# Optimization experiments

Measured on AMD Instinct MI355X. Metric: run time of the kernel, lower is better.

Reference implementation:

```python
import jax, jax.numpy as jnp
import numpy as np
from jax import lax

D_MODEL = 768
N_LAYER = 4
VOCAB = 50280  # 50277 padded to multiple of 8
D_INNER = 2 * D_MODEL
D_STATE = 16
D_CONV = 4
DT_RANK = 48  # ceil(768/16)
EPS = 1e-5


def setup_inputs() -> dict:
    key = jax.random.key(0)
    ks = iter(jax.random.split(key, 16))
    s = 0.02
    B, L = 1, 1024
    inp = {
        "input_ids": jax.random.randint(next(ks), (B, L), 0, 50277, dtype=jnp.int64).astype(jnp.int32),
        "embedding": jax.random.normal(next(ks), (VOCAB, D_MODEL), jnp.float32) * s,
        "in_proj_w": jax.random.normal(next(ks), (N_LAYER, 2 * D_INNER, D_MODEL), jnp.float32) * s,
        "conv_w": jax.random.normal(next(ks), (N_LAYER, D_INNER, 1, D_CONV), jnp.float32) * s,
        "conv_b": jnp.zeros((N_LAYER, D_INNER), jnp.float32),
        "x_proj_w": jax.random.normal(next(ks), (N_LAYER, DT_RANK + 2 * D_STATE, D_INNER), jnp.float32) * s,
        "dt_proj_w": jax.random.normal(next(ks), (N_LAYER, D_INNER, DT_RANK), jnp.float32) * s,
        "dt_proj_b": jax.random.uniform(next(ks), (N_LAYER, D_INNER), jnp.float32, -4.0, -2.0),
        "A_log": jnp.log(jnp.broadcast_to(jnp.arange(1, D_STATE + 1, dtype=jnp.float32), (N_LAYER, D_INNER, D_STATE))),
        "D_param": jnp.ones((N_LAYER, D_INNER), jnp.float32),
        "out_proj_w": jax.random.normal(next(ks), (N_LAYER, D_MODEL, D_INNER), jnp.float32) * s,
        "norm_w": jnp.ones((N_LAYER, D_MODEL), jnp.float32),
        "norm_f_w": jnp.ones((D_MODEL,), jnp.float32),
    }
    return inp


def rmsnorm(x, w):
    var = jnp.mean(jnp.square(x), axis=-1, keepdims=True)
    return x * lax.rsqrt(var + EPS) * w


def silu(x):
    return x * jax.nn.sigmoid(x)


def mamba_mixer(h, in_w, cw, cb, xw, dtw, dtb, A_log, Dp, ow):
    B, L, _ = h.shape
    xz = jnp.einsum("bld,ed->ble", h, in_w)          # [B,L,2*d_inner]
    x, z = jnp.split(xz, 2, axis=-1)
    # causal depthwise conv1d over length
    xc = lax.conv_general_dilated(
        x.transpose(0, 2, 1), cw, (1,), [(D_CONV - 1, 0)],
        dimension_numbers=("NCH", "OIH", "NCH"), feature_group_count=D_INNER,
    ).transpose(0, 2, 1) + cb                          # [B,L,d_inner]
    xc = silu(xc)
    dbl = jnp.einsum("bld,ed->ble", xc, xw)            # [B,L,R+2N]
    dt = jax.nn.softplus(jnp.einsum("blr,dr->bld", dbl[..., :DT_RANK], dtw) + dtb)
    Bm = dbl[..., DT_RANK:DT_RANK + D_STATE]           # [B,L,N]
    Cm = dbl[..., DT_RANK + D_STATE:]                  # [B,L,N]
    A = -jnp.exp(A_log)                                # [d_inner,N]
    dA = jnp.exp(dt[..., None] * A)                    # [B,L,d_inner,N]
    dBx = dt[..., None] * Bm[:, :, None, :] * xc[..., None]

    def step(s, inp):
        a, b, c = inp
        s = a * s + b
        y = jnp.einsum("bdn,bn->bd", s, c)
        return s, y

    s0 = jnp.zeros((B, D_INNER, D_STATE), h.dtype)
    _, ys = lax.scan(step, s0, (dA.transpose(1, 0, 2, 3), dBx.transpose(1, 0, 2, 3), Cm.transpose(1, 0, 2)))
    y = ys.transpose(1, 0, 2) + xc * Dp                # [B,L,d_inner]
    y = y * silu(z)
    return jnp.einsum("ble,de->bld", y, ow)


def reference(input_ids, embedding, in_proj_w, conv_w, conv_b, x_proj_w,
              dt_proj_w, dt_proj_b, A_log, D_param, out_proj_w, norm_w, norm_f_w):
    h = embedding[input_ids]                           # [B,L,D]
    for i in range(N_LAYER):
        h = h + mamba_mixer(rmsnorm(h, norm_w[i]), in_proj_w[i], conv_w[i], conv_b[i],
                            x_proj_w[i], dt_proj_w[i], dt_proj_b[i], A_log[i],
                            D_param[i], out_proj_w[i])
    h = rmsnorm(h, norm_f_w)
    logits = jnp.einsum("bld,vd->blv", h, embedding)   # tied lm_head
    return logits
```

## Files before the change

kernel.cpp:

```cpp
#include <hip/hip_runtime.h>
#include <cstdint>
#include <cstddef>

#define N_LAYER 4
#define VOCABSZ 50280
#define VOCABPAD 50304
#define DMODEL 768
#define DINNER 1536
#define DSTATE 16
#define DTRANK 48
#define SEQL 1024

typedef __bf16 bf16x8 __attribute__((ext_vector_type(8)));
typedef unsigned short us8 __attribute__((ext_vector_type(8)));
typedef float f32x4 __attribute__((ext_vector_type(4)));

__device__ __forceinline__ unsigned short f2bf(float f) {
    unsigned int u = __builtin_bit_cast(unsigned int, f);
    u = (u + 0x7FFFu + ((u >> 16) & 1u)) >> 16;
    return (unsigned short)u;
}

__device__ __forceinline__ void glds16(const unsigned short* g, unsigned short* l) {
    __builtin_amdgcn_global_load_lds(
        (const __attribute__((address_space(1))) void*)g,
        (__attribute__((address_space(3))) void*)l, 16, 0, 0);
}

__global__ __launch_bounds__(256) void cvt_bf16_kernel(
    const float* __restrict__ src, unsigned short* __restrict__ dst, int n8)
{
    int i = blockIdx.x * 256 + threadIdx.x;
    if (i >= n8) return;
    const float4* s = (const float4*)src + (size_t)i * 2;
    float4 a = s[0], b = s[1];
    us8 o = { f2bf(a.x), f2bf(a.y), f2bf(a.z), f2bf(a.w),
              f2bf(b.x), f2bf(b.y), f2bf(b.z), f2bf(b.w) };
    *(us8*)(dst + (size_t)i * 8) = o;
}

__global__ __launch_bounds__(256) void cvt_xw_kernel(
    const float* __restrict__ xw, unsigned short* __restrict__ xwB)
{
    int g = blockIdx.x * 256 + threadIdx.x;
    if (g >= N_LAYER * 128 * 192) return;
    int row = g / 192;
    int c8  = g % 192;
    int layer = row >> 7;
    int r = row & 127;
    us8 o;
    if (r < 80) {
        const float4* s = (const float4*)(xw + ((size_t)(layer * 80 + r) * DINNER) + c8 * 8);
        float4 a = s[0], b = s[1];
        o = (us8){ f2bf(a.x), f2bf(a.y), f2bf(a.z), f2bf(a.w),
                   f2bf(b.x), f2bf(b.y), f2bf(b.z), f2bf(b.w) };
    } else {
        o = (us8){0, 0, 0, 0, 0, 0, 0, 0};
    }
    *(us8*)(xwB + (size_t)row * DINNER + c8 * 8) = o;
}

__device__ __forceinline__ void gemm_compute32(
    const unsigned short* sAbuf, const unsigned short* sBbuf,
    int wm, int wn, int frs, f32x4 (&acc)[4][4])
{
    bf16x8 af[4], bfr[4];
#pragma unroll
    for (int t = 0; t < 4; ++t) {
        af[t]  = __builtin_bit_cast(bf16x8, *(const us8*)&sAbuf[(wm + t * 16) * 32 + frs]);
        bfr[t] = __builtin_bit_cast(bf16x8, *(const us8*)&sBbuf[(wn + t * 16) * 32 + frs]);
    }
#pragma unroll
    for (int mt = 0; mt < 4; ++mt)
#pragma unroll
        for (int nt = 0; nt < 4; ++nt)
            acc[mt][nt] = __builtin_amdgcn_mfma_f32_16x16x32_bf16(
                af[mt], bfr[nt], acc[mt][nt], 0, 0, 0);
}

template <int ADD>
__device__ __forceinline__ void gemm_bf_body(
    const unsigned short* __restrict__ A, const unsigned short* __restrict__ B,
    const float* __restrict__ ADDSRC, float* __restrict__ C, int N, int K)
{
    __shared__ unsigned short sA0[128 * 32];
    __shared__ unsigned short sA1[128 * 32];
    __shared__ unsigned short sB0[128 * 32];
    __shared__ unsigned short sB1[128 * 32];

    const int tid  = threadIdx.x;
    const int lane = tid & 63;
    const int wave = tid >> 6;
    const int wm = (wave & 1) * 64;
    const int wn = (wave >> 1) * 64;
    const int bid = blockIdx.x;
    const int cpx = (int)gridDim.x >> 3;
    const int swz = (bid & 7) * cpx + (bid >> 3);
    const int bm = (swz & 7) << 7;
    const int bn = (swz >> 3) << 7;

    const int scol = ((tid & 3) ^ ((tid >> 3) & 3)) * 8;
    const unsigned short* Ag0 = A + (size_t)(bm + (tid >> 2)) * K + scol;
    const unsigned short* Ag1 = Ag0 + (size_t)64 * K;
    const unsigned short* Bg0 = B + (size_t)(bn + (tid >> 2)) * K + scol;
    const unsigned short* Bg1 = Bg0 + (size_t)64 * K;
    unsigned short* lA0a = sA0 + tid * 8;  unsigned short* lA0b = lA0a + 2048;
    unsigned short* lA1a = sA1 + tid * 8;  unsigned short* lA1b = lA1a + 2048;
    unsigned short* lB0a = sB0 + tid * 8;  unsigned short* lB0b = lB0a + 2048;
    unsigned short* lB1a = sB1 + tid * 8;  unsigned short* lB1b = lB1a + 2048;

    f32x4 acc[4][4];
#pragma unroll
    for (int i = 0; i < 4; ++i)
#pragma unroll
        for (int j = 0; j < 4; ++j) acc[i][j] = (f32x4){0.f, 0.f, 0.f, 0.f};

    const int frs = (lane & 15) * 32 + (((lane >> 4) ^ ((lane >> 1) & 3))) * 8;

    glds16(Ag0, lA0a); glds16(Ag1, lA0b);
    glds16(Bg0, lB0a); glds16(Bg1, lB0b);
    Ag0 += 32; Ag1 += 32; Bg0 += 32; Bg1 += 32;
    __syncthreads();

    for (int k0 = 0; k0 < K; k0 += 64) {
        glds16(Ag0, lA1a); glds16(Ag1, lA1b);
        glds16(Bg0, lB1a); glds16(Bg1, lB1b);
        Ag0 += 32; Ag1 += 32; Bg0 += 32; Bg1 += 32;
        gemm_compute32(sA0, sB0, wm, wn, frs, acc);
        __syncthreads();

        if (k0 + 64 < K) {
            glds16(Ag0, lA0a); glds16(Ag1, lA0b);
            glds16(Bg0, lB0a); glds16(Bg1, lB0b);
            Ag0 += 32; Ag1 += 32; Bg0 += 32; Bg1 += 32;
        }
        gemm_compute32(sA1, sB1, wm, wn, frs, acc);
        __syncthreads();
    }

    const int cn = lane & 15;
    const int cm = (lane >> 4) * 4;
#pragma unroll
    for (int mt = 0; mt < 4; ++mt) {
#pragma unroll
        for (int nt = 0; nt < 4; ++nt) {
            int n = bn + wn + nt * 16 + cn;
            if (n < N) {
#pragma unroll
                for (int r = 0; r < 4; ++r) {
                    int m = bm + wm + mt * 16 + cm + r;
                    size_t idx = (size_t)m * N + n;
                    float v = acc[mt][nt][r];
                    if constexpr (ADD) v += ADDSRC[idx];
                    C[idx] = v;
                }
            }
        }
    }
}

__global__ __launch_bounds__(256) void gemm_in_kernel(
    const unsigned short* __restrict__ A, const unsigned short* __restrict__ B,
    float* __restrict__ C, int N, int K)
{ gemm_bf_body<0>(A, B, nullptr, C, N, K); }

__global__ __launch_bounds__(256) void gemm_out_kernel(
    const unsigned short* __restrict__ A, const unsigned short* __restrict__ B,
    const float* __restrict__ ADDSRC, float* __restrict__ C, int N, int K)
{ gemm_bf_body<1>(A, B, ADDSRC, C, N, K); }

__global__ __launch_bounds__(256) void gemm_xproj_kernel(
    const unsigned short* __restrict__ A, const unsigned short* __restrict__ B,
    float* __restrict__ C, int N, int K)
{ gemm_bf_body<0>(A, B, nullptr, C, N, K); }

__global__ __launch_bounds__(256) void gemm_logits_kernel(
    const unsigned short* __restrict__ A, const unsigned short* __restrict__ B,
    float* __restrict__ C, int N, int K)
{ gemm_bf_body<0>(A, B, nullptr, C, N, K); }

template <int ADD>
__global__ __launch_bounds__(256) void gemm_fb_kernel(
    const float* __restrict__ A, const float* __restrict__ B,
    const float* __restrict__ ADDSRC, float* __restrict__ C,
    int N, int K)
{
    __shared__ unsigned short sA[128 * 40];
    __shared__ unsigned short sB[128 * 40];
    const int tid  = threadIdx.x;
    const int lane = tid & 63;
    const int wave = tid >> 6;
    const int wm = (wave & 1) * 64;
    const int wn = (wave >> 1) * 64;
    const int bm = blockIdx.y * 128;
    const int bn = blockIdx.x * 128;
    const int srow = tid >> 1;
    const int scol = (tid & 1) * 16;
    const float* Ap = A + (size_t)(bm + srow) * K + scol;
    const int brow  = bn + srow;
    const bool bvalid = brow < N;
    const float* Bp = B + (size_t)(bvalid ? brow : 0) * K + scol;
    f32x4 acc[4][4];
#pragma unroll
    for (int i = 0; i < 4; ++i)
#pragma unroll
        for (int j = 0; j < 4; ++j) acc[i][j] = (f32x4){0.f, 0.f, 0.f, 0.f};
    unsigned short* sAp = &sA[srow * 40 + scol];
    unsigned short* sBp = &sB[srow * 40 + scol];
    const int fr = (lane & 15) * 40 + (lane >> 4) * 8;
    for (int k0 = 0; k0 < K; k0 += 32) {
        float4 a0 = *(const float4*)(Ap + k0);
        float4 a1 = *(const float4*)(Ap + k0 + 4);
        float4 a2 = *(const float4*)(Ap + k0 + 8);
        float4 a3 = *(const float4*)(Ap + k0 + 12);
        float4 b0, b1, b2, b3;
        if (bvalid) {
            b0 = *(const float4*)(Bp + k0);
            b1 = *(const float4*)(Bp + k0 + 4);
            b2 = *(const float4*)(Bp + k0 + 8);
            b3 = *(const float4*)(Bp + k0 + 12);
        } else {
            b0 = make_float4(0.f, 0.f, 0.f, 0.f);
            b1 = b0; b2 = b0; b3 = b0;
        }
        __syncthreads();
        us8 va0 = { f2bf(a0.x), f2bf(a0.y), f2bf(a0.z), f2bf(a0.w),
                    f2bf(a1.x), f2bf(a1.y), f2bf(a1.z), f2bf(a1.w) };
        us8 va1 = { f2bf(a2.x), f2bf(a2.y), f2bf(a2.z), f2bf(a2.w),
                    f2bf(a3.x), f2bf(a3.y), f2bf(a3.z), f2bf(a3.w) };
        us8 vb0 = { f2bf(b0.x), f2bf(b0.y), f2bf(b0.z), f2bf(b0.w),
                    f2bf(b1.x), f2bf(b1.y), f2bf(b1.z), f2bf(b1.w) };
        us8 vb1 = { f2bf(b2.x), f2bf(b2.y), f2bf(b2.z), f2bf(b2.w),
                    f2bf(b3.x), f2bf(b3.y), f2bf(b3.z), f2bf(b3.w) };
        *(us8*)(sAp)     = va0;
        *(us8*)(sAp + 8) = va1;
        *(us8*)(sBp)     = vb0;
        *(us8*)(sBp + 8) = vb1;
        __syncthreads();
        bf16x8 af[4], bfr[4];
#pragma unroll
        for (int t = 0; t < 4; ++t) {
            af[t]  = __builtin_bit_cast(bf16x8, *(const us8*)&sA[wm * 40 + t * 640 + fr]);
            bfr[t] = __builtin_bit_cast(bf16x8, *(const us8*)&sB[wn * 40 + t * 640 + fr]);
        }
#pragma unroll
        for (int mt = 0; mt < 4; ++mt)
#pragma unroll
            for (int nt = 0; nt < 4; ++nt)
                acc[mt][nt] = __builtin_amdgcn_mfma_f32_16x16x32_bf16(
                    af[mt], bfr[nt], acc[mt][nt], 0, 0, 0);
    }
    const int cn = lane & 15;
    const int cm = (lane >> 4) * 4;
#pragma unroll
    for (int mt = 0; mt < 4; ++mt) {
#pragma unroll
        for (int nt = 0; nt < 4; ++nt) {
            int n = bn + wn + nt * 16 + cn;
            if (n < N) {
#pragma unroll
                for (int r = 0; r < 4; ++r) {
                    int m = bm + wm + mt * 16 + cm + r;
                    size_t idx = (size_t)m * N + n;
                    float v = acc[mt][nt][r];
                    if constexpr (ADD) v += ADDSRC[idx];
                    C[idx] = v;
                }
            }
        }
    }
}

__global__ __launch_bounds__(256) void embed_kernel(
    const int* __restrict__ ids, const float* __restrict__ emb, float* __restrict__ h)
{
    int l = blockIdx.x;
    int id = ids[l];
    const float* src = emb + (size_t)id * DMODEL;
    for (int d = threadIdx.x; d < DMODEL; d += 256) h[(size_t)l * DMODEL + d] = src[d];
}

template <typename OT>
__global__ __launch_bounds__(256) void rmsnorm_kernel(
    const float* __restrict__ x, const float* __restrict__ w,
    OT* __restrict__ out, int D)
{
    int l = blockIdx.x;
    const float* xr = x + (size_t)l * D;
    float ss = 0.f;
    for (int d = threadIdx.x; d < D; d += 256) { float v = xr[d]; ss += v * v; }
#pragma unroll
    for (int off = 32; off > 0; off >>= 1) ss += __shfl_down(ss, off, 64);
    __shared__ float red[4];
    __shared__ float invs;
    if ((threadIdx.x & 63) == 0) red[threadIdx.x >> 6] = ss;
    __syncthreads();
    if (threadIdx.x == 0)
        invs = rsqrtf((red[0] + red[1] + red[2] + red[3]) / (float)D + 1e-5f);
    __syncthreads();
    float inv = invs;
    for (int d = threadIdx.x; d < D; d += 256) {
        float v = xr[d] * inv * w[d];
        if constexpr (sizeof(OT) == 2) out[(size_t)l * D + d] = f2bf(v);
        else                           out[(size_t)l * D + d] = v;
    }
}

__global__ __launch_bounds__(256) void conv_silu_kernel(
    const float* __restrict__ xz, const float* __restrict__ cw,
    const float* __restrict__ cb, float* __restrict__ xc,
    unsigned short* __restrict__ xcB)
{
    int l = blockIdx.x / 6;
    int d = (blockIdx.x % 6) * 256 + threadIdx.x;
    float w0 = cw[d * 4], w1 = cw[d * 4 + 1], w2 = cw[d * 4 + 2], w3 = cw[d * 4 + 3];
    float acc = cb[d];
    if (l >= 3) acc += xz[(size_t)(l - 3) * 3072 + d] * w0;
    if (l >= 2) acc += xz[(size_t)(l - 2) * 3072 + d] * w1;
    if (l >= 1) acc += xz[(size_t)(l - 1) * 3072 + d] * w2;
    acc += xz[(size_t)l * 3072 + d] * w3;
    float sig = 1.f / (1.f + __expf(-acc));
    float v = acc * sig;
    size_t idx = (size_t)l * DINNER + d;
    xc[idx]  = v;
    xcB[idx] = f2bf(v);
}

__global__ __launch_bounds__(256) void xproj_kernel(
    const float* __restrict__ xc, const float* __restrict__ xw, float* __restrict__ dbl)
{
    int l = blockIdx.x;
    __shared__ float sx[DINNER];
    for (int d = threadIdx.x; d < DINNER; d += 256) sx[d] = xc[(size_t)l * DINNER + d];
    __syncthreads();
    int wave = threadIdx.x >> 6, lane = threadIdx.x & 63;
    for (int e = wave * 20; e < wave * 20 + 20; ++e) {
        const float* wr = xw + (size_t)e * DINNER;
        float s = 0.f;
        for (int d = lane; d < DINNER; d += 64) s += sx[d] * wr[d];
#pragma unroll
        for (int off = 32; off > 0; off >>= 1) s += __shfl_down(s, off, 64);
        if (lane == 0) dbl[l * 80 + e] = s;
    }
}

__global__ __launch_bounds__(256) void dtproj_kernel(
    const float* __restrict__ dbl, const float* __restrict__ dtw,
    const float* __restrict__ dtb, float* __restrict__ dt)
{
    int l = blockIdx.x / 6;
    int e = (blockIdx.x % 6) * 256 + threadIdx.x;
    __shared__ float sd[48];
    if (threadIdx.x < 48) sd[threadIdx.x] = dbl[l * 80 + threadIdx.x];
    __syncthreads();
    float a = dtb[e];
    const float4* wr = (const float4*)(dtw + (size_t)e * 48);
#pragma unroll
    for (int q = 0; q < 12; ++q) {
        float4 w4 = wr[q];
        a += sd[q * 4] * w4.x + sd[q * 4 + 1] * w4.y + sd[q * 4 + 2] * w4.z + sd[q * 4 + 3] * w4.w;
    }
    dt[(size_t)l * DINNER + e] = (a > 20.f) ? a : log1pf(__expf(a));
}

template <typename OT>
__global__ __launch_bounds__(64) void scan_kernel(
    const float* __restrict__ dt, const float* __restrict__ dbl,
    const float* __restrict__ xc, const float* __restrict__ xz,
    const float* __restrict__ alog, const float* __restrict__ dpar,
    OT* __restrict__ yf)
{
    int d0 = blockIdx.x * 4;
    int lane = threadIdx.x;
    int n = lane & 15;
    int dloc = lane >> 4;
    int d = d0 + dloc;
    float A = -__expf(alog[d * 16 + n]);
    float Dq[4];
#pragma unroll
    for (int q = 0; q < 4; ++q) Dq[q] = dpar[d0 + q];

    __shared__ float sdt[64][4];
    __shared__ float sxc[64][4];
    __shared__ float sz[64][4];
    __shared__ float sB[64][16];
    __shared__ float sC[64][16];
    __shared__ float pp[4][64][17];

    float s = 0.f;
    for (int c0 = 0; c0 < SEQL; c0 += 64) {
        int l = c0 + lane;
        *(float4*)&sdt[lane][0] = *(const float4*)&dt[(size_t)l * DINNER + d0];
        *(float4*)&sxc[lane][0] = *(const float4*)&xc[(size_t)l * DINNER + d0];
        *(float4*)&sz[lane][0]  = *(const float4*)&xz[(size_t)l * 3072 + DINNER + d0];
#pragma unroll
        for (int q = 0; q < 4; ++q) {
            *(float4*)&sB[lane][q * 4] = *(const float4*)&dbl[l * 80 + 48 + q * 4];
            *(float4*)&sC[lane][q * 4] = *(const float4*)&dbl[l * 80 + 64 + q * 4];
        }
        __syncthreads();
#pragma unroll 4
        for (int j = 0; j < 64; ++j) {
            float dtv = sdt[j][dloc];
            float xv  = sxc[j][dloc];
            float a = __expf(dtv * A);
            s = fmaf(a, s, dtv * sB[j][n] * xv);
            pp[dloc][j][n] = s * sC[j][n];
        }
        __syncthreads();
#pragma unroll
        for (int q = 0; q < 4; ++q) {
            float accv = 0.f;
#pragma unroll
            for (int nn = 0; nn < 16; ++nn) accv += pp[q][lane][nn];
            float xv = sxc[lane][q];
            float zv = sz[lane][q];
            float sig = 1.f / (1.f + __expf(-zv));
            float v = (accv + xv * Dq[q]) * (zv * sig);
            if constexpr (sizeof(OT) == 2) yf[(size_t)(c0 + lane) * DINNER + d0 + q] = f2bf(v);
            else                           yf[(size_t)(c0 + lane) * DINNER + d0 + q] = v;
        }
        __syncthreads();
    }
}

extern "C" void kernel_launch(void* const* d_in, const int* in_sizes, int n_in,
                              void* d_out, int out_size, void* d_ws, size_t ws_size,
                              hipStream_t stream)
{
    const int*   ids  = (const int*)d_in[0];
    const float* emb  = (const float*)d_in[1];
    const float* inw  = (const float*)d_in[2];
    const float* cw   = (const float*)d_in[3];
    const float* cb   = (const float*)d_in[4];
    const float* xw   = (const float*)d_in[5];
    const float* dtw  = (const float*)d_in[6];
    const float* dtb  = (const float*)d_in[7];
    const float* alog = (const float*)d_in[8];
    const float* dpar = (const float*)d_in[9];
    const float* ow   = (const float*)d_in[10];
    const float* nw   = (const float*)d_in[11];
    const float* nfw  = (const float*)d_in[12];
    float* out = (float*)d_out;

    const size_t MAIN_WS = 138936320ull;

    if (ws_size >= MAIN_WS) {
        char* p = (char*)d_ws;
        float* h    = (float*)p;                 p += (size_t)SEQL * DMODEL * 4;
        float* xz   = (float*)p;                 p += (size_t)SEQL * 3072 * 4;
        float* xc   = (float*)p;                 p += (size_t)SEQL * DINNER * 4;
        float* dbl  = (float*)p;                 p += (size_t)SEQL * 80 * 4;
        float* dt   = (float*)p;                 p += (size_t)SEQL * DINNER * 4;
        unsigned short* xnB  = (unsigned short*)p; p += (size_t)SEQL * DMODEL * 2;
        unsigned short* yfB  = (unsigned short*)p; p += (size_t)SEQL * DINNER * 2;
        unsigned short* embB = (unsigned short*)p; p += (size_t)VOCABPAD * DMODEL * 2;
        unsigned short* inwB = (unsigned short*)p; p += (size_t)N_LAYER * 3072 * DMODEL * 2;
        unsigned short* owB  = (unsigned short*)p; p += (size_t)N_LAYER * DMODEL * DINNER * 2;

        unsigned short* xwB = (unsigned short*)out;
        unsigned short* xcB = xwB + (size_t)N_LAYER * 128 * DINNER;

        int n8;
        n8 = VOCABSZ * DMODEL / 8;
        cvt_bf16_kernel<<<(n8 + 255) / 256, 256, 0, stream>>>(emb, embB, n8);
        n8 = N_LAYER * 3072 * DMODEL / 8;
        cvt_bf16_kernel<<<(n8 + 255) / 256, 256, 0, stream>>>(inw, inwB, n8);
        n8 = N_LAYER * DMODEL * DINNER / 8;
        cvt_bf16_kernel<<<(n8 + 255) / 256, 256, 0, stream>>>(ow, owB, n8);
        cvt_xw_kernel<<<(N_LAYER * 128 * 192 + 255) / 256, 256, 0, stream>>>(xw, xwB);

        embed_kernel<<<SEQL, 256, 0, stream>>>(ids, emb, h);

        for (int i = 0; i < N_LAYER; ++i) {
            rmsnorm_kernel<unsigned short><<<SEQL, 256, 0, stream>>>(
                h, nw + (size_t)i * DMODEL, xnB, DMODEL);
            gemm_in_kernel<<<8 * (3072 / 128), 256, 0, stream>>>(
                xnB, inwB + (size_t)i * 3072 * DMODEL, xz, 3072, DMODEL);
            conv_silu_kernel<<<SEQL * 6, 256, 0, stream>>>(
                xz, cw + (size_t)i * DINNER * 4, cb + (size_t)i * DINNER, xc, xcB);
            gemm_xproj_kernel<<<8, 256, 0, stream>>>(
                xcB, xwB + (size_t)i * 128 * DINNER, dbl, 80, DINNER);
            dtproj_kernel<<<SEQL * 6, 256, 0, stream>>>(
                dbl, dtw + (size_t)i * DINNER * DTRANK, dtb + (size_t)i * DINNER, dt);
            scan_kernel<unsigned short><<<DINNER / 4, 64, 0, stream>>>(
                dt, dbl, xc, xz, alog + (size_t)i * DINNER * DSTATE,
                dpar + (size_t)i * DINNER, yfB);
            gemm_out_kernel<<<8 * (DMODEL / 128), 256, 0, stream>>>(
                yfB, owB + (size_t)i * DMODEL * DINNER, h, h, DMODEL, DINNER);
        }

        rmsnorm_kernel<unsigned short><<<SEQL, 256, 0, stream>>>(h, nfw, xnB, DMODEL);
        gemm_logits_kernel<<<8 * ((VOCABSZ + 127) / 128), 256, 0, stream>>>(
            xnB, embB, out, VOCABSZ, DMODEL);
    } else {
        float* h   = (float*)d_ws;
        float* xn  = h  + (size_t)SEQL * DMODEL;
        float* xz  = xn + (size_t)SEQL * DMODEL;
        float* xc  = xz + (size_t)SEQL * 3072;
        float* dbl = xc + (size_t)SEQL * DINNER;
        float* dt  = dbl + (size_t)SEQL * 80;
        float* yf  = dt + (size_t)SEQL * DINNER;
        unsigned short* xcB = (unsigned short*)out;

        embed_kernel<<<SEQL, 256, 0, stream>>>(ids, emb, h);
        for (int i = 0; i < N_LAYER; ++i) {
            rmsnorm_kernel<float><<<SEQL, 256, 0, stream>>>(h, nw + (size_t)i * DMODEL, xn, DMODEL);
            gemm_fb_kernel<0><<<dim3(3072 / 128, SEQL / 128), 256, 0, stream>>>(
                xn, inw + (size_t)i * 3072 * DMODEL, nullptr, xz, 3072, DMODEL);
            conv_silu_kernel<<<SEQL * 6, 256, 0, stream>>>(
                xz, cw + (size_t)i * DINNER * 4, cb + (size_t)i * DINNER, xc, xcB);
            xproj_kernel<<<SEQL, 256, 0, stream>>>(xc, xw + (size_t)i * 80 * DINNER, dbl);
            dtproj_kernel<<<SEQL * 6, 256, 0, stream>>>(
                dbl, dtw + (size_t)i * DINNER * DTRANK, dtb + (size_t)i * DINNER, dt);
            scan_kernel<float><<<DINNER / 4, 64, 0, stream>>>(
                dt, dbl, xc, xz, alog + (size_t)i * DINNER * DSTATE, dpar + (size_t)i * DINNER, yf);
            gemm_fb_kernel<1><<<dim3(DMODEL / 128, SEQL / 128), 256, 0, stream>>>(
                yf, ow + (size_t)i * DMODEL * DINNER, h, h, DMODEL, DINNER);
        }
        rmsnorm_kernel<float><<<SEQL, 256, 0, stream>>>(h, nfw, xn, DMODEL);
        gemm_fb_kernel<0><<<dim3((VOCABSZ + 127) / 128, SEQL / 128), 256, 0, stream>>>(
            xn, emb, nullptr, out, VOCABSZ, DMODEL);
    }
}
```

Before: 1.221 ms.

## Split-K out_proj, fuse residual into rmsnorm, fuse dt_proj into scan, merge casts

The out_proj GEMM is now split four ways along K so 192 blocks run instead of 48. Partial sums go to a scratch buffer, and a new rmsnorm_acc kernel adds them into h and normalizes in one pass. The dt projection and softplus are computed inside the scan kernel from the x_proj output, which removes the separate dtproj kernel and its dt round trip to memory. The three weight conversions are merged into one launch. The cost is extra partial-sum traffic and extra per-block dt arithmetic inside the serial scan.

```diff
diff --git a/kernel.cpp b/kernel.cpp
--- a/kernel.cpp
+++ b/kernel.cpp
@@ -10,6 +10,7 @@
 #define DSTATE 16
 #define DTRANK 48
 #define SEQL 1024
+#define HPSTRIDE (SEQL * DMODEL)
 
 typedef __bf16 bf16x8 __attribute__((ext_vector_type(8)));
 typedef unsigned short us8 __attribute__((ext_vector_type(8)));
@@ -27,16 +28,40 @@
         (__attribute__((address_space(3))) void*)l, 16, 0, 0);
 }
 
+__device__ __forceinline__ void cvt8(const float* s, unsigned short* d) {
+    const float4* s4 = (const float4*)s;
+    float4 a = s4[0], b = s4[1];
+    us8 o = { f2bf(a.x), f2bf(a.y), f2bf(a.z), f2bf(a.w),
+              f2bf(b.x), f2bf(b.y), f2bf(b.z), f2bf(b.w) };
+    *(us8*)d = o;
+}
+
 __global__ __launch_bounds__(256) void cvt_bf16_kernel(
     const float* __restrict__ src, unsigned short* __restrict__ dst, int n8)
 {
     int i = blockIdx.x * 256 + threadIdx.x;
     if (i >= n8) return;
-    const float4* s = (const float4*)src + (size_t)i * 2;
-    float4 a = s[0], b = s[1];
-    us8 o = { f2bf(a.x), f2bf(a.y), f2bf(a.z), f2bf(a.w),
-              f2bf(b.x), f2bf(b.y), f2bf(b.z), f2bf(b.w) };
-    *(us8*)(dst + (size_t)i * 8) = o;
+    cvt8(src + (size_t)i * 8, dst + (size_t)i * 8);
+}
+
+__global__ __launch_bounds__(256) void cvt3_kernel(
+    const float* __restrict__ s0, unsigned short* __restrict__ d0, int n0,
+    const float* __restrict__ s1, unsigned short* __restrict__ d1, int n1,
+    const float* __restrict__ s2, unsigned short* __restrict__ d2, int n2)
+{
+    int i = blockIdx.x * 256 + threadIdx.x;
+    const float* s; unsigned short* d; int j = i;
+    if (j < n0) { s = s0; d = d0; }
+    else {
+        j -= n0;
+        if (j < n1) { s = s1; d = d1; }
+        else {
+            j -= n1;
+            if (j >= n2) return;
+            s = s2; d = d2;
+        }
+    }
+    cvt8(s + (size_t)j * 8, d + (size_t)j * 8);
 }
 
 __global__ __launch_bounds__(256) void cvt_xw_kernel(
@@ -78,10 +103,9 @@
                 af[mt], bfr[nt], acc[mt][nt], 0, 0, 0);
 }
 
-template <int ADD>
-__device__ __forceinline__ void gemm_bf_body(
+__device__ __forceinline__ void gemm_core(
     const unsigned short* __restrict__ A, const unsigned short* __restrict__ B,
-    const float* __restrict__ ADDSRC, float* __restrict__ C, int N, int K)
+    float* __restrict__ C, int N, int Kstride, int Klen, int bm, int bn)
 {
     __shared__ unsigned short sA0[128 * 32];
     __shared__ unsigned short sA1[128 * 32];
@@ -93,17 +117,12 @@
     const int wave = tid >> 6;
     const int wm = (wave & 1) * 64;
     const int wn = (wave >> 1) * 64;
-    const int bid = blockIdx.x;
-    const int cpx = (int)gridDim.x >> 3;
-    const int swz = (bid & 7) * cpx + (bid >> 3);
-    const int bm = (swz & 7) << 7;
-    const int bn = (swz >> 3) << 7;
 
     const int scol = ((tid & 3) ^ ((tid >> 3) & 3)) * 8;
-    const unsigned short* Ag0 = A + (size_t)(bm + (tid >> 2)) * K + scol;
-    const unsigned short* Ag1 = Ag0 + (size_t)64 * K;
-    const unsigned short* Bg0 = B + (size_t)(bn + (tid >> 2)) * K + scol;
-    const unsigned short* Bg1 = Bg0 + (size_t)64 * K;
+    const unsigned short* Ag0 = A + (size_t)(bm + (tid >> 2)) * Kstride + scol;
+    const unsigned short* Ag1 = Ag0 + (size_t)64 * Kstride;
+    const unsigned short* Bg0 = B + (size_t)(bn + (tid >> 2)) * Kstride + scol;
+    const unsigned short* Bg1 = Bg0 + (size_t)64 * Kstride;
     unsigned short* lA0a = sA0 + tid * 8;  unsigned short* lA0b = lA0a + 2048;
     unsigned short* lA1a = sA1 + tid * 8;  unsigned short* lA1b = lA1a + 2048;
     unsigned short* lB0a = sB0 + tid * 8;  unsigned short* lB0b = lB0a + 2048;
@@ -122,14 +141,14 @@
     Ag0 += 32; Ag1 += 32; Bg0 += 32; Bg1 += 32;
     __syncthreads();
 
-    for (int k0 = 0; k0 < K; k0 += 64) {
+    for (int k0 = 0; k0 < Klen; k0 += 64) {
         glds16(Ag0, lA1a); glds16(Ag1, lA1b);
         glds16(Bg0, lB1a); glds16(Bg1, lB1b);
         Ag0 += 32; Ag1 += 32; Bg0 += 32; Bg1 += 32;
         gemm_compute32(sA0, sB0, wm, wn, frs, acc);
         __syncthreads();
 
-        if (k0 + 64 < K) {
+        if (k0 + 64 < Klen) {
             glds16(Ag0, lA0a); glds16(Ag1, lA0b);
             glds16(Bg0, lB0a); glds16(Bg1, lB0b);
             Ag0 += 32; Ag1 += 32; Bg0 += 32; Bg1 += 32;
@@ -149,35 +168,50 @@
 #pragma unroll
                 for (int r = 0; r < 4; ++r) {
                     int m = bm + wm + mt * 16 + cm + r;
-                    size_t idx = (size_t)m * N + n;
-                    float v = acc[mt][nt][r];
-                    if constexpr (ADD) v += ADDSRC[idx];
-                    C[idx] = v;
+                    C[(size_t)m * N + n] = acc[mt][nt][r];
                 }
             }
         }
     }
+}
+
+__device__ __forceinline__ void swz_mn(int bid, int grid, int& bm, int& bn)
+{
+    int cpx = grid >> 3;
+    int swz = (bid & 7) * cpx + (bid >> 3);
+    bm = (swz & 7) << 7;
+    bn = (swz >> 3) << 7;
 }
 
 __global__ __launch_bounds__(256) void gemm_in_kernel(
     const unsigned short* __restrict__ A, const unsigned short* __restrict__ B,
     float* __restrict__ C, int N, int K)
-{ gemm_bf_body<0>(A, B, nullptr, C, N, K); }
-
-__global__ __launch_bounds__(256) void gemm_out_kernel(
-    const unsigned short* __restrict__ A, const unsigned short* __restrict__ B,
-    const float* __restrict__ ADDSRC, float* __restrict__ C, int N, int K)
-{ gemm_bf_body<1>(A, B, ADDSRC, C, N, K); }
+{ int bm, bn; swz_mn(blockIdx.x, gridDim.x, bm, bn); gemm_core(A, B, C, N, K, K, bm, bn); }
 
 __global__ __launch_bounds__(256) void gemm_xproj_kernel(
     const unsigned short* __restrict__ A, const unsigned short* __restrict__ B,
     float* __restrict__ C, int N, int K)
-{ gemm_bf_body<0>(A, B, nullptr, C, N, K); }
+{ int bm, bn; swz_mn(blockIdx.x, gridDim.x, bm, bn); gemm_core(A, B, C, N, K, K, bm, bn); }
 
 __global__ __launch_bounds__(256) void gemm_logits_kernel(
     const unsigned short* __restrict__ A, const unsigned short* __restrict__ B,
     float* __restrict__ C, int N, int K)
-{ gemm_bf_body<0>(A, B, nullptr, C, N, K); }
+{ int bm, bn; swz_mn(blockIdx.x, gridDim.x, bm, bn); gemm_core(A, B, C, N, K, K, bm, bn); }
+
+__global__ __launch_bounds__(256) void gemm_outp_kernel(
+    const unsigned short* __restrict__ A, const unsigned short* __restrict__ B,
+    float* __restrict__ hp, int N, int Kstride, int Klen)
+{
+    int bid = blockIdx.x;
+    int split = bid / 48;
+    int r = bid - split * 48;
+    int swz = (r & 7) * 6 + (r >> 3);
+    int bm = (swz & 7) << 7;
+    int bn = (swz >> 3) << 7;
+    int kbase = split * Klen;
+    gemm_core(A + kbase, B + kbase, hp + (size_t)split * HPSTRIDE,
+              N, Kstride, Klen, bm, bn);
+}
 
 template <int ADD>
 __global__ __launch_bounds__(256) void gemm_fb_kernel(
@@ -306,6 +340,38 @@
     }
 }
 
+__global__ __launch_bounds__(256) void rmsnorm_acc_kernel(
+    float* __restrict__ h, const float* __restrict__ hp,
+    const float* __restrict__ w, unsigned short* __restrict__ out)
+{
+    int l = blockIdx.x;
+    const size_t base = (size_t)l * DMODEL;
+    __shared__ float row[DMODEL];
+    float ss = 0.f;
+    for (int d = threadIdx.x; d < DMODEL; d += 256) {
+        float v = h[base + d]
+                + hp[base + d]
+                + hp[base + d + (size_t)HPSTRIDE]
+                + hp[base + d + (size_t)2 * HPSTRIDE]
+                + hp[base + d + (size_t)3 * HPSTRIDE];
+        row[d] = v;
+        h[base + d] = v;
+        ss += v * v;
+    }
+#pragma unroll
+    for (int off = 32; off > 0; off >>= 1) ss += __shfl_down(ss, off, 64);
+    __shared__ float red[4];
+    __shared__ float invs;
+    if ((threadIdx.x & 63) == 0) red[threadIdx.x >> 6] = ss;
+    __syncthreads();
+    if (threadIdx.x == 0)
+        invs = rsqrtf((red[0] + red[1] + red[2] + red[3]) / (float)DMODEL + 1e-5f);
+    __syncthreads();
+    float inv = invs;
+    for (int d = threadIdx.x; d < DMODEL; d += 256)
+        out[base + d] = f2bf(row[d] * inv * w[d]);
+}
+
 __global__ __launch_bounds__(256) void conv_silu_kernel(
     const float* __restrict__ xz, const float* __restrict__ cw,
     const float* __restrict__ cb, float* __restrict__ xc,
@@ -419,6 +485,83 @@
             float v = (accv + xv * Dq[q]) * (zv * sig);
             if constexpr (sizeof(OT) == 2) yf[(size_t)(c0 + lane) * DINNER + d0 + q] = f2bf(v);
             else                           yf[(size_t)(c0 + lane) * DINNER + d0 + q] = v;
+        }
+        __syncthreads();
+    }
+}
+
+__global__ __launch_bounds__(64) void scan_fused_kernel(
+    const float* __restrict__ dbl, const float* __restrict__ xc,
+    const float* __restrict__ xz, const float* __restrict__ dtw,
+    const float* __restrict__ dtb, const float* __restrict__ alog,
+    const float* __restrict__ dpar, unsigned short* __restrict__ yf)
+{
+    int d0 = blockIdx.x * 4;
+    int lane = threadIdx.x;
+    int n = lane & 15;
+    int dloc = lane >> 4;
+    int d = d0 + dloc;
+    float A = -__expf(alog[d * 16 + n]);
+    float Dq[4], dtbq[4];
+#pragma unroll
+    for (int q = 0; q < 4; ++q) { Dq[q] = dpar[d0 + q]; dtbq[q] = dtb[d0 + q]; }
+
+    __shared__ float swt[4][48];
+    for (int t = lane; t < 192; t += 64)
+        swt[t / 48][t % 48] = dtw[(size_t)(d0 + t / 48) * 48 + t % 48];
+
+    __shared__ float sdt[64][4];
+    __shared__ float sxc[64][4];
+    __shared__ float sz[64][4];
+    __shared__ float sB[64][16];
+    __shared__ float sC[64][16];
+    __shared__ float pp[4][64][17];
+    __syncthreads();
+
+    float s = 0.f;
+    for (int c0 = 0; c0 < SEQL; c0 += 64) {
+        int l = c0 + lane;
+        *(float4*)&sxc[lane][0] = *(const float4*)&xc[(size_t)l * DINNER + d0];
+        *(float4*)&sz[lane][0]  = *(const float4*)&xz[(size_t)l * 3072 + DINNER + d0];
+        float4 db[12];
+#pragma unroll
+        for (int q4 = 0; q4 < 12; ++q4)
+            db[q4] = *(const float4*)&dbl[l * 80 + q4 * 4];
+#pragma unroll
+        for (int q = 0; q < 4; ++q) {
+            *(float4*)&sB[lane][q * 4] = *(const float4*)&dbl[l * 80 + 48 + q * 4];
+            *(float4*)&sC[lane][q * 4] = *(const float4*)&dbl[l * 80 + 64 + q * 4];
+        }
+#pragma unroll
+        for (int q = 0; q < 4; ++q) {
+            float a = dtbq[q];
+#pragma unroll
+            for (int q4 = 0; q4 < 12; ++q4) {
+                float4 w4 = *(const float4*)&swt[q][q4 * 4];
+                a += db[q4].x * w4.x + db[q4].y * w4.y + db[q4].z * w4.z + db[q4].w * w4.w;
+            }
+            sdt[lane][q] = (a > 20.f) ? a : log1pf(__expf(a));
+        }
+        __syncthreads();
+#pragma unroll 4
+        for (int j = 0; j < 64; ++j) {
+            float dtv = sdt[j][dloc];
+            float xv  = sxc[j][dloc];
+            float a = __expf(dtv * A);
+            s = fmaf(a, s, dtv * sB[j][n] * xv);
+            pp[dloc][j][n] = s * sC[j][n];
+        }
+        __syncthreads();
+#pragma unroll
+        for (int q = 0; q < 4; ++q) {
+            float accv = 0.f;
+#pragma unroll
+            for (int nn = 0; nn < 16; ++nn) accv += pp[q][lane][nn];
+            float xv = sxc[lane][q];
+            float zv = sz[lane][q];
+            float sig = 1.f / (1.f + __expf(-zv));
+            float v = (accv + xv * Dq[q]) * (zv * sig);
+            yf[(size_t)(c0 + lane) * DINNER + d0 + q] = f2bf(v);
         }
         __syncthreads();
     }
@@ -451,46 +594,49 @@
         float* xz   = (float*)p;                 p += (size_t)SEQL * 3072 * 4;
         float* xc   = (float*)p;                 p += (size_t)SEQL * DINNER * 4;
         float* dbl  = (float*)p;                 p += (size_t)SEQL * 80 * 4;
-        float* dt   = (float*)p;                 p += (size_t)SEQL * DINNER * 4;
+        float* dt_unused = (float*)p;            p += (size_t)SEQL * DINNER * 4;
         unsigned short* xnB  = (unsigned short*)p; p += (size_t)SEQL * DMODEL * 2;
         unsigned short* yfB  = (unsigned short*)p; p += (size_t)SEQL * DINNER * 2;
         unsigned short* embB = (unsigned short*)p; p += (size_t)VOCABPAD * DMODEL * 2;
         unsigned short* inwB = (unsigned short*)p; p += (size_t)N_LAYER * 3072 * DMODEL * 2;
         unsigned short* owB  = (unsigned short*)p; p += (size_t)N_LAYER * DMODEL * DINNER * 2;
+        (void)dt_unused;
 
         unsigned short* xwB = (unsigned short*)out;
         unsigned short* xcB = xwB + (size_t)N_LAYER * 128 * DINNER;
-
-        int n8;
-        n8 = VOCABSZ * DMODEL / 8;
-        cvt_bf16_kernel<<<(n8 + 255) / 256, 256, 0, stream>>>(emb, embB, n8);
-        n8 = N_LAYER * 3072 * DMODEL / 8;
-        cvt_bf16_kernel<<<(n8 + 255) / 256, 256, 0, stream>>>(inw, inwB, n8);
-        n8 = N_LAYER * DMODEL * DINNER / 8;
-        cvt_bf16_kernel<<<(n8 + 255) / 256, 256, 0, stream>>>(ow, owB, n8);
+        float* hp = (float*)(xcB + (size_t)SEQL * DINNER);
+
+        const int n0 = VOCABSZ * DMODEL / 8;
+        const int n1 = N_LAYER * 3072 * DMODEL / 8;
+        const int n2 = N_LAYER * DMODEL * DINNER / 8;
+        cvt3_kernel<<<(n0 + n1 + n2 + 255) / 256, 256, 0, stream>>>(
+            emb, embB, n0, inw, inwB, n1, ow, owB, n2);
         cvt_xw_kernel<<<(N_LAYER * 128 * 192 + 255) / 256, 256, 0, stream>>>(xw, xwB);
 
         embed_kernel<<<SEQL, 256, 0, stream>>>(ids, emb, h);
 
         for (int i = 0; i < N_LAYER; ++i) {
-            rmsnorm_kernel<unsigned short><<<SEQL, 256, 0, stream>>>(
-                h, nw + (size_t)i * DMODEL, xnB, DMODEL);
+            if (i == 0)
+                rmsnorm_kernel<unsigned short><<<SEQL, 256, 0, stream>>>(
+                    h, nw, xnB, DMODEL);
+            else
+                rmsnorm_acc_kernel<<<SEQL, 256, 0, stream>>>(
+                    h, hp, nw + (size_t)i * DMODEL, xnB);
             gemm_in_kernel<<<8 * (3072 / 128), 256, 0, stream>>>(
                 xnB, inwB + (size_t)i * 3072 * DMODEL, xz, 3072, DMODEL);
             conv_silu_kernel<<<SEQL * 6, 256, 0, stream>>>(
                 xz, cw + (size_t)i * DINNER * 4, cb + (size_t)i * DINNER, xc, xcB);
             gemm_xproj_kernel<<<8, 256, 0, stream>>>(
                 xcB, xwB + (size_t)i * 128 * DINNER, dbl, 80, DINNER);
-            dtproj_kernel<<<SEQL * 6, 256, 0, stream>>>(
-                dbl, dtw + (size_t)i * DINNER * DTRANK, dtb + (size_t)i * DINNER, dt);
-            scan_kernel<unsigned short><<<DINNER / 4, 64, 0, stream>>>(
-                dt, dbl, xc, xz, alog + (size_t)i * DINNER * DSTATE,
+            scan_fused_kernel<<<DINNER / 4, 64, 0, stream>>>(
+                dbl, xc, xz, dtw + (size_t)i * DINNER * DTRANK,
+                dtb + (size_t)i * DINNER, alog + (size_t)i * DINNER * DSTATE,
                 dpar + (size_t)i * DINNER, yfB);
-            gemm_out_kernel<<<8 * (DMODEL / 128), 256, 0, stream>>>(
-                yfB, owB + (size_t)i * DMODEL * DINNER, h, h, DMODEL, DINNER);
-        }
-
-        rmsnorm_kernel<unsigned short><<<SEQL, 256, 0, stream>>>(h, nfw, xnB, DMODEL);
+            gemm_outp_kernel<<<4 * 48, 256, 0, stream>>>(
+                yfB, owB + (size_t)i * DMODEL * DINNER, hp, DMODEL, DINNER, DINNER / 4);
+        }
+
+        rmsnorm_acc_kernel<<<SEQL, 256, 0, stream>>>(h, hp, nfw, xnB);
         gemm_logits_kernel<<<8 * ((VOCABSZ + 127) / 128), 256, 0, stream>>>(
             xnB, embB, out, VOCABSZ, DMODEL);
     } else {
```

Result: no change. 1.199 ms (-1.8%).
